# Kernel tuning notes

Hardware: AMD Instinct MI355X
Metric: run time of the kernel (lower is better)

The kernel has to match this reference:

```python
import jax, jax.numpy as jnp
import numpy as np
import math
from functools import lru_cache

# ---------- Clebsch-Gordan machinery (numpy, setup-time only) ----------

def _cg(j1, m1, j2, m2, j, m):
    """Complex-basis CG coefficient via Racah's formula (Condon-Shortley)."""
    if m1 + m2 != m:
        return 0.0
    f = math.factorial
    pre = (2 * j + 1) * f(j1 + j2 - j) * f(j1 - j2 + j) * f(-j1 + j2 + j) / f(j1 + j2 + j + 1)
    pre *= f(j1 + m1) * f(j1 - m1) * f(j2 + m2) * f(j2 - m2) * f(j + m) * f(j - m)
    s = 0.0
    for k in range(0, j1 + j2 - j + 1):
        d = (k, j1 + j2 - j - k, j1 - m1 - k, j2 + m2 - k, j - j2 + m1 + k, j - j1 - m2 + k)
        if min(d) < 0:
            continue
        s += (-1) ** k / (f(d[0]) * f(d[1]) * f(d[2]) * f(d[3]) * f(d[4]) * f(d[5]))
    return math.sqrt(pre) * s


def _csh_to_rsh(j):
    """Unitary complex->real spherical harmonics transform, columns indexed by real m."""
    C = np.zeros((2 * j + 1, 2 * j + 1), dtype=np.complex128)
    s2 = 1.0 / math.sqrt(2.0)
    for m in range(-j, j + 1):
        am = abs(m)
        if m < 0:
            C[j + m, j + m] = 1j * s2
            C[j - m, j + m] = -1j * ((-1) ** am) * s2
        elif m == 0:
            C[j, j] = 1.0
        else:
            C[j - m, j + m] = s2
            C[j + m, j + m] = ((-1) ** am) * s2
    return C


@lru_cache(maxsize=None)
def _rsh_cg(j1, j2, j):
    """Real-basis CG, compactified to rows [m1, m2, m, coeff] over nonzeros."""
    csh = np.zeros((2 * j1 + 1, 2 * j2 + 1, 2 * j + 1), dtype=np.complex128)
    for m1 in range(-j1, j1 + 1):
        for m2 in range(-j2, j2 + 1):
            m = m1 + m2
            if -j <= m <= j:
                csh[j1 + m1, j2 + m2, j + m] = _cg(j1, m1, j2, m2, j, m)
    r = np.einsum('abc,ai,bj,ck->ijk', csh, _csh_to_rsh(j1), _csh_to_rsh(j2), np.conj(_csh_to_rsh(j)))
    r = np.real(r * ((-1j) ** (j1 + j2 + j)))
    m1g, m2g, mg = np.meshgrid(np.arange(-j1, j1 + 1), np.arange(-j2, j2 + 1),
                               np.arange(-j, j + 1), indexing='ij')
    mask = np.abs(r) > 1e-12
    return np.stack([m1g[mask].astype(np.float64), m2g[mask].astype(np.float64),
                     mg[mask].astype(np.float64), r[mask]], axis=0)


def _build_coupler(md1, md2, trunc_in=True):
    """Faithful replay of CGPCoupler._init_params: returns cg_tilde, repids, out_dim."""
    md1 = np.asarray(md1, dtype=np.int64)
    md2 = np.asarray(md2, dtype=np.int64)
    md_in = np.stack([md1, md2], axis=0)                      # [2, 2*(L+1)]
    max_n_out = np.maximum(md1, md2)
    nlp = md_in.shape[1]
    n_irr = np.repeat(np.arange(nlp // 2) * 2 + 1, 2)         # irreps per (l,p) slot
    off_in = np.cumsum(md_in * n_irr[None, :], axis=1)
    off_in = np.concatenate([np.zeros((2, 1), dtype=np.int64), off_in[:, :-1]], axis=1)
    max_l = nlp // 2 - 1
    md_out = np.zeros_like(max_n_out)
    valid = []
    for lout in range(max_l + 1):
        for pout in (1, -1):
            for l1 in range(max_l + 1):
                for l2 in range(max_l + 1):
                    for p1 in (1, -1):
                        for p2 in (1, -1):
                            cp = (-1) ** (lout + l1 + l2)
                            if p1 * p2 * cp != pout:
                                continue
                            if l1 + l2 < lout or abs(l1 - l2) > lout:
                                continue
                            lp1 = 2 * l1 + (1 - p1) // 2
                            lp2 = 2 * l2 + (1 - p2) // 2
                            lpo = 2 * lout + (1 - pout) // 2
                            if trunc_in:
                                if l1 + l2 > max_l:
                                    continue
                                deg = min(md_in[0, lp1], md_in[1, lp2],
                                          max_n_out[2 * (l1 + l2) + (1 - pout) // 2])
                            else:
                                deg = min(md_in[0, lp1], md_in[1, lp2], max_n_out[lpo])
                            md_out[lpo] += deg
                            if deg > 0:
                                valid.append((lpo, lp1, lp2, int(deg)))
    off_out = np.cumsum(md_out * n_irr)
    off_out = np.concatenate([[0], off_out[:-1]]).astype(np.int64)
    cg_l, r1_l, r2_l, ro_l = [], [], [], []
    ns_off, lpo_last = 0, 0
    for lpo, lp1, lp2, deg in valid:
        if lpo > lpo_last:
            ns_off = 0
        l1, l2, lout = lp1 // 2, lp2 // 2, lpo // 2
        src = _rsh_cg(l1, l2, lout)                            # [4, nnz]
        seg = np.repeat(src, deg, axis=1)                      # repeat_interleave along dim=1
        ns = np.tile(np.arange(deg, dtype=np.int64), src.shape[1])
        r1_l.append(off_in[0, lp1] + np.rint(seg[0] + l1).astype(np.int64) * md_in[0, lp1] + ns)
        r2_l.append(off_in[1, lp2] + np.rint(seg[1] + l2).astype(np.int64) * md_in[1, lp2] + ns)
        ro_l.append(off_out[lpo] + np.rint(seg[2] + lout).astype(np.int64) * md_out[lpo] + ns_off + ns)
        cg_l.append(seg[3])
        ns_off += deg
        lpo_last = lpo
    out_dim = int(np.sum(md_out * n_irr))
    return (np.concatenate(cg_l), np.concatenate(r1_l), np.concatenate(r2_l),
            np.concatenate(ro_l), out_dim)


METADATA = [32, 32, 32, 32, 32, 32, 32, 32]   # max_l = 3, 32 channels per (l, parity)
BATCH = 2048


def setup_inputs() -> dict:
    key = jax.random.key(0)
    k1, k2 = jax.random.split(key)
    cg, r1, r2, ro, out_dim = _build_coupler(METADATA, METADATA, trunc_in=True)
    n_irr = np.repeat(np.arange(len(METADATA) // 2) * 2 + 1, 2)
    in_dim = int(np.sum(np.asarray(METADATA) * n_irr))        # 1024
    x1 = jax.random.normal(k1, (BATCH, in_dim), dtype=jnp.float32)
    x2 = jax.random.normal(k2, (BATCH, in_dim), dtype=jnp.float32)
    return {
        "x1": x1,
        "x2": x2,
        "cg_tilde": jnp.asarray(cg, dtype=jnp.float32),
        "repids_in1": jnp.asarray(r1, dtype=jnp.int64) if jax.config.jax_enable_x64 else jnp.asarray(r1, dtype=jnp.int32),
        "repids_in2": jnp.asarray(r2, dtype=jnp.int64) if jax.config.jax_enable_x64 else jnp.asarray(r2, dtype=jnp.int32),
        "repids_out": jnp.asarray(ro, dtype=jnp.int64) if jax.config.jax_enable_x64 else jnp.asarray(ro, dtype=jnp.int32),
        "out_dim": out_dim,
    }


def reference(x1, x2, cg_tilde, repids_in1, repids_in2, repids_out, out_dim):
    # gather along rep dim (last), elementwise multiply with CG coeffs, scatter-add
    out_tilde = x1[:, repids_in1] * x2[:, repids_in2] * cg_tilde[None, :]   # [B, K]
    out = jnp.zeros((x1.shape[0], out_dim), dtype=x1.dtype).at[:, repids_out].add(out_tilde)
    return out
```

## Files before the change

### kernel.cpp

```cpp
#include <hip/hip_runtime.h>


#define IN_DIM  1024
#define ROWS    8
#define NOBCAP  512
#define SKIP_OB 511u

__global__ __launch_bounds__(1024) void prep_kernel(
    const int* __restrict__ r1, const int* __restrict__ r2,
    const int* __restrict__ ro, const float* __restrict__ cg,
    int nseg, int nob,
    uint2* __restrict__ qdesc, uint2* __restrict__ ddesc, uint2* __restrict__ sdesc,
    int* __restrict__ zlist, int* __restrict__ hdr)
{
    __shared__ int cntS[NOBCAP], rankS[NOBCAP];
    __shared__ int qoffS[NOBCAP], doffS[NOBCAP], soffS[NOBCAP];
    __shared__ unsigned long long wsumS[8], woffS[8];
    const int t = threadIdx.x;

    if (t < NOBCAP) { cntS[t] = 0; rankS[t] = 0; }
    __syncthreads();

    for (int s = t; s < nseg; s += 1024)
        atomicAdd(&cntS[ro[s << 5] >> 5], 1);
    __syncthreads();

    int c = 0;
    unsigned long long pv = 0ull;
    if (t < NOBCAP) {
        c = (t < nob) ? cntS[t] : 0;
        unsigned long long q = 0, df = 0, sf = 0, zf = 0;
        if (t < nob) {
            if (c == 2)      df = 1;
            else if (c <= 1) sf = 1;
            else { q = (unsigned long long)((c + 3) >> 2); if (c > 4) zf = 1; }
        }
        pv = (q << 48) | (df << 32) | (sf << 16) | zf;
    }
    const int lane = t & 63;
    const int wid  = t >> 6;
    #pragma unroll
    for (int off = 1; off < 64; off <<= 1) {
        const unsigned long long n = __shfl_up(pv, off, 64);
        if (lane >= off) pv += n;
    }
    if (t < NOBCAP && lane == 63) wsumS[wid] = pv;
    __syncthreads();
    if (t < 8) {
        unsigned long long v = wsumS[t];
        const unsigned long long self = v;
        #pragma unroll
        for (int off = 1; off < 8; off <<= 1) {
            const unsigned long long n = __shfl_up(v, off, 64);
            if (t >= off) v += n;
        }
        woffS[t] = v - self;
    }
    __syncthreads();

    if (t < NOBCAP) {
        const unsigned long long incl = pv + woffS[wid];
        const int qi = (int)(incl >> 48);
        const int di = (int)((incl >> 32) & 0xFFFFull);
        const int si = (int)((incl >> 16) & 0xFFFFull);
        const int zi = (int)(incl & 0xFFFFull);
        if (t < nob) {
            if (c == 2) {
                doffS[t] = di - 1;
            } else if (c <= 1) {
                soffS[t] = si - 1;
                if (c == 0)
                    sdesc[si - 1] = make_uint2(((unsigned int)t << 20) | 0x80000000u, 0u);
            } else {
                const int qn = (c + 3) >> 2;
                const int qb = qi - qn;
                qoffS[t] = qb;
                const unsigned int fl = (c > 4) ? 0u : 0x80000000u;
                if (c > 4) zlist[zi - 1] = t;
                const unsigned int pd = ((unsigned int)t << 20) | fl;
                for (int j = (qb << 2) + c; j < ((qb + qn) << 2); ++j)
                    qdesc[j] = make_uint2(pd, 0u);
            }
        }
        if (t == NOBCAP - 1) {
            const int nq = qi, nd = di, ns = si;
            const int nqPad = (nq + 15) & ~15;
            const int ndPad = (nd + 31) & ~31;
            const int nsPad = (ns + 63) & ~63;
            const uint2 dummy = make_uint2(SKIP_OB << 20, 0u);
            for (int j = (nq << 2); j < (nqPad << 2); ++j) qdesc[j] = dummy;
            for (int j = (nd << 1); j < (ndPad << 1); ++j) ddesc[j] = dummy;
            for (int j = ns;        j < nsPad;        ++j) sdesc[j] = dummy;
            hdr[0] = nqPad; hdr[1] = zi; hdr[2] = ndPad; hdr[3] = nsPad;
        }
    }
    __syncthreads();

    for (int s = t; s < nseg; s += 1024) {
        const int k  = s << 5;
        const int ob = ro[k] >> 5;
        const int cc = cntS[ob];
        const int rk = atomicAdd(&rankS[ob], 1);
        const unsigned int fl = (cc > 4) ? 0u : 0x80000000u;
        const uint2 v = make_uint2((unsigned int)r1[k] | ((unsigned int)r2[k] << 10)
                                   | ((unsigned int)ob << 20) | fl,
                                   __float_as_uint(cg[k]));
        if (cc == 2)      ddesc[(doffS[ob] << 1) + rk] = v;
        else if (cc == 1) sdesc[soffS[ob]] = v;
        else              qdesc[(qoffS[ob] << 2) + rk] = v;
    }
}

__device__ __forceinline__ void accum4(float4& acc, unsigned int dx, unsigned int dc,
                                       const float* xs1, const float* xs2)
{
    const float  c = __uint_as_float(dc);
    const float4 u = *reinterpret_cast<const float4*>(xs1 + (dx & 1023u));
    const float4 v = *reinterpret_cast<const float4*>(xs2 + ((dx >> 10) & 1023u));
    acc.x = fmaf(c, u.x * v.x, acc.x);
    acc.y = fmaf(c, u.y * v.y, acc.y);
    acc.z = fmaf(c, u.z * v.z, acc.z);
    acc.w = fmaf(c, u.w * v.w, acc.w);
}

__device__ __forceinline__ void terminal(float* orow, unsigned int hx, float4 acc)
{
    const int ob = (int)((hx >> 20) & 511u);
    if (ob == (int)SKIP_OB) return;
    float* p = orow + (ob << 5);
    if (hx >> 31) {
        *reinterpret_cast<float4*>(p) = acc;
    } else {
        unsafeAtomicAdd(p,     acc.x);
        unsafeAtomicAdd(p + 1, acc.y);
        unsafeAtomicAdd(p + 2, acc.z);
        unsafeAtomicAdd(p + 3, acc.w);
    }
}

__global__ __launch_bounds__(1024) void cgp_main(const float* __restrict__ x1,
    const float* __restrict__ x2, const uint2* __restrict__ qdesc,
    const uint2* __restrict__ ddesc, const uint2* __restrict__ sdesc,
    const int* __restrict__ zlist, const int* __restrict__ hdr,
    float* __restrict__ out, int out_dim)
{
    __shared__ float x1s[ROWS * IN_DIM];
    __shared__ float x2s[ROWS * IN_DIM];
    const int r0  = blockIdx.x * ROWS;
    const int tid = threadIdx.x;

    {
        const float4* p1 = reinterpret_cast<const float4*>(x1 + (size_t)r0 * IN_DIM);
        const float4* p2 = reinterpret_cast<const float4*>(x2 + (size_t)r0 * IN_DIM);
        float4* s1 = reinterpret_cast<float4*>(x1s);
        float4* s2 = reinterpret_cast<float4*>(x2s);
        #pragma unroll
        for (int j = tid; j < (ROWS * IN_DIM) >> 2; j += 1024) { s1[j] = p1[j]; s2[j] = p2[j]; }
    }
    const int nz = hdr[1];
    for (int i = tid; i < (nz << 5); i += 1024) {
        const int ob = zlist[i >> 5];
        const int ch = i & 31;
        float* p = out + (size_t)r0 * out_dim + (ob << 5) + ch;
        #pragma unroll
        for (int j = 0; j < ROWS; ++j) p[j * out_dim] = 0.f;
    }
    __syncthreads();

    const int w  = tid >> 6;
    const int ln = tid & 63;
    const int rr = ln >> 3;
    const int tt = ln & 7;
    const float* xs1 = x1s + rr * IN_DIM + (tt << 2);
    const float* xs2 = x2s + rr * IN_DIM + (tt << 2);
    float* orow = out + (size_t)(r0 + rr) * out_dim + (tt << 2);

    {
        const int qpw = hdr[0] >> 4;
        const uint2* qd = qdesc + ((size_t)(w * qpw) << 2);
        #pragma unroll 2
        for (int i = 0; i < qpw; ++i, qd += 4) {
            const uint4 A  = *reinterpret_cast<const uint4*>(qd);
            const uint4 Bq = *reinterpret_cast<const uint4*>(qd + 2);
            float4 acc = make_float4(0.f, 0.f, 0.f, 0.f);
            accum4(acc, A.x,  A.y,  xs1, xs2);
            accum4(acc, A.z,  A.w,  xs1, xs2);
            accum4(acc, Bq.x, Bq.y, xs1, xs2);
            accum4(acc, Bq.z, Bq.w, xs1, xs2);
            terminal(orow, A.x, acc);
        }
    }

    {
        const int ppw = hdr[2] >> 5;
        const uint2* dd = ddesc + ((size_t)(w * ppw) << 2);
        #pragma unroll 2
        for (int i = 0; i < ppw; ++i, dd += 4) {
            const uint4 A  = *reinterpret_cast<const uint4*>(dd);
            const uint4 Bq = *reinterpret_cast<const uint4*>(dd + 2);
            float4 a0 = make_float4(0.f, 0.f, 0.f, 0.f);
            float4 a1 = make_float4(0.f, 0.f, 0.f, 0.f);
            accum4(a0, A.x,  A.y,  xs1, xs2);
            accum4(a0, A.z,  A.w,  xs1, xs2);
            accum4(a1, Bq.x, Bq.y, xs1, xs2);
            accum4(a1, Bq.z, Bq.w, xs1, xs2);
            terminal(orow, A.x,  a0);
            terminal(orow, Bq.x, a1);
        }
    }

    {
        const int spw = hdr[3] >> 4;
        const int ipw = spw >> 2;
        const uint2* sd = sdesc + (size_t)(w * spw);
        #pragma unroll 2
        for (int i = 0; i < ipw; ++i, sd += 4) {
            const uint4 A  = *reinterpret_cast<const uint4*>(sd);
            const uint4 Bq = *reinterpret_cast<const uint4*>(sd + 2);
            float4 a0 = make_float4(0.f, 0.f, 0.f, 0.f);
            float4 a1 = make_float4(0.f, 0.f, 0.f, 0.f);
            float4 a2 = make_float4(0.f, 0.f, 0.f, 0.f);
            float4 a3 = make_float4(0.f, 0.f, 0.f, 0.f);
            accum4(a0, A.x,  A.y,  xs1, xs2);
            accum4(a1, A.z,  A.w,  xs1, xs2);
            accum4(a2, Bq.x, Bq.y, xs1, xs2);
            accum4(a3, Bq.z, Bq.w, xs1, xs2);
            terminal(orow, A.x,  a0);
            terminal(orow, A.z,  a1);
            terminal(orow, Bq.x, a2);
            terminal(orow, Bq.z, a3);
        }
    }
}

extern "C" void kernel_launch(void* const* d_in, const int* in_sizes, int n_in,
                              void* d_out, int out_size, void* d_ws, size_t ws_size,
                              hipStream_t stream)
{
    const float* x1 = (const float*)d_in[0];
    const float* x2 = (const float*)d_in[1];
    const float* cg = (const float*)d_in[2];
    const int*   r1 = (const int*)d_in[3];
    const int*   r2 = (const int*)d_in[4];
    const int*   ro = (const int*)d_in[5];
    float* out = (float*)d_out;

    const int B       = in_sizes[0] / IN_DIM;
    const int out_dim = out_size / B;
    const int K       = in_sizes[2];
    const int nseg    = K >> 5;
    const int nob     = out_dim >> 5;
    const int qcap    = nob + (nseg >> 2) + 32;
    const int dcap    = nob + 48;
    const int scap    = nob + 80;

    auto align16 = [](size_t v) { return (v + 15) & ~(size_t)15; };
    char* ws = (char*)d_ws;
    uint2* qdesc = (uint2*)ws;  ws += align16((size_t)qcap * 4 * sizeof(uint2));
    uint2* ddesc = (uint2*)ws;  ws += align16((size_t)dcap * 2 * sizeof(uint2));
    uint2* sdesc = (uint2*)ws;  ws += align16((size_t)scap * sizeof(uint2));
    int*   zlist = (int*)ws;    ws += align16((size_t)NOBCAP * sizeof(int));
    int*   hdr   = (int*)ws;

    hipLaunchKernelGGL(prep_kernel, dim3(1), dim3(1024), 0, stream,
                       r1, r2, ro, cg, nseg, nob, qdesc, ddesc, sdesc, zlist, hdr);
    hipLaunchKernelGGL(cgp_main, dim3(B / ROWS), dim3(1024), 0, stream,
                       x1, x2, qdesc, ddesc, sdesc, zlist, hdr, out, out_dim);
}
```

Measured before the change: 28.87 us.

## Halve rows per block and split each wave into two half-waves on different descriptors

```diff
diff --git a/kernel.cpp b/kernel.cpp
--- a/kernel.cpp
+++ b/kernel.cpp
@@ -2,7 +2,7 @@
 
 
 #define IN_DIM  1024
-#define ROWS    8
+#define ROWS    4
 #define NOBCAP  512
 #define SKIP_OB 511u
 
@@ -138,7 +138,7 @@
     }
 }
 
-__global__ __launch_bounds__(1024) void cgp_main(const float* __restrict__ x1,
+__global__ __launch_bounds__(512) void cgp_main(const float* __restrict__ x1,
     const float* __restrict__ x2, const uint2* __restrict__ qdesc,
     const uint2* __restrict__ ddesc, const uint2* __restrict__ sdesc,
     const int* __restrict__ zlist, const int* __restrict__ hdr,
@@ -155,10 +155,10 @@
         float4* s1 = reinterpret_cast<float4*>(x1s);
         float4* s2 = reinterpret_cast<float4*>(x2s);
         #pragma unroll
-        for (int j = tid; j < (ROWS * IN_DIM) >> 2; j += 1024) { s1[j] = p1[j]; s2[j] = p2[j]; }
+        for (int j = tid; j < (ROWS * IN_DIM) >> 2; j += 512) { s1[j] = p1[j]; s2[j] = p2[j]; }
     }
     const int nz = hdr[1];
-    for (int i = tid; i < (nz << 5); i += 1024) {
+    for (int i = tid; i < (nz << 5); i += 512) {
         const int ob = zlist[i >> 5];
         const int ch = i & 31;
         float* p = out + (size_t)r0 * out_dim + (ob << 5) + ch;
@@ -169,19 +169,24 @@
 
     const int w  = tid >> 6;
     const int ln = tid & 63;
-    const int rr = ln >> 3;
-    const int tt = ln & 7;
+    const bool hi = (ln >> 5) != 0;
+    const int hl = ln & 31;
+    const int rr = hl >> 3;
+    const int tt = hl & 7;
     const float* xs1 = x1s + rr * IN_DIM + (tt << 2);
     const float* xs2 = x2s + rr * IN_DIM + (tt << 2);
     float* orow = out + (size_t)(r0 + rr) * out_dim + (tt << 2);
 
     {
-        const int qpw = hdr[0] >> 4;
+        const int qpw = hdr[0] >> 3;
         const uint2* qd = qdesc + ((size_t)(w * qpw) << 2);
-        #pragma unroll 2
-        for (int i = 0; i < qpw; ++i, qd += 4) {
-            const uint4 A  = *reinterpret_cast<const uint4*>(qd);
-            const uint4 Bq = *reinterpret_cast<const uint4*>(qd + 2);
+        for (int i = 0; i < qpw; i += 2, qd += 8) {
+            const uint4 A0 = *reinterpret_cast<const uint4*>(qd);
+            const uint4 B0 = *reinterpret_cast<const uint4*>(qd + 2);
+            const uint4 A1 = *reinterpret_cast<const uint4*>(qd + 4);
+            const uint4 B1 = *reinterpret_cast<const uint4*>(qd + 6);
+            const uint4 A  = hi ? A1 : A0;
+            const uint4 Bq = hi ? B1 : B0;
             float4 acc = make_float4(0.f, 0.f, 0.f, 0.f);
             accum4(acc, A.x,  A.y,  xs1, xs2);
             accum4(acc, A.z,  A.w,  xs1, xs2);
@@ -192,12 +197,15 @@
     }
 
     {
-        const int ppw = hdr[2] >> 5;
-        const uint2* dd = ddesc + ((size_t)(w * ppw) << 2);
-        #pragma unroll 2
-        for (int i = 0; i < ppw; ++i, dd += 4) {
-            const uint4 A  = *reinterpret_cast<const uint4*>(dd);
-            const uint4 Bq = *reinterpret_cast<const uint4*>(dd + 2);
+        const int dpw = hdr[2] >> 3;
+        const uint2* dd = ddesc + ((size_t)(w * dpw) << 1);
+        for (int i = 0; i < dpw; i += 4, dd += 8) {
+            const uint4 A0 = *reinterpret_cast<const uint4*>(dd);
+            const uint4 B0 = *reinterpret_cast<const uint4*>(dd + 2);
+            const uint4 A1 = *reinterpret_cast<const uint4*>(dd + 4);
+            const uint4 B1 = *reinterpret_cast<const uint4*>(dd + 6);
+            const uint4 A  = hi ? A1 : A0;
+            const uint4 Bq = hi ? B1 : B0;
             float4 a0 = make_float4(0.f, 0.f, 0.f, 0.f);
             float4 a1 = make_float4(0.f, 0.f, 0.f, 0.f);
             accum4(a0, A.x,  A.y,  xs1, xs2);
@@ -210,13 +218,15 @@
     }
 
     {
-        const int spw = hdr[3] >> 4;
-        const int ipw = spw >> 2;
+        const int spw = hdr[3] >> 3;
         const uint2* sd = sdesc + (size_t)(w * spw);
-        #pragma unroll 2
-        for (int i = 0; i < ipw; ++i, sd += 4) {
-            const uint4 A  = *reinterpret_cast<const uint4*>(sd);
-            const uint4 Bq = *reinterpret_cast<const uint4*>(sd + 2);
+        for (int i = 0; i < spw; i += 8, sd += 8) {
+            const uint4 A0 = *reinterpret_cast<const uint4*>(sd);
+            const uint4 B0 = *reinterpret_cast<const uint4*>(sd + 2);
+            const uint4 A1 = *reinterpret_cast<const uint4*>(sd + 4);
+            const uint4 B1 = *reinterpret_cast<const uint4*>(sd + 6);
+            const uint4 A  = hi ? A1 : A0;
+            const uint4 Bq = hi ? B1 : B0;
             float4 a0 = make_float4(0.f, 0.f, 0.f, 0.f);
             float4 a1 = make_float4(0.f, 0.f, 0.f, 0.f);
             float4 a2 = make_float4(0.f, 0.f, 0.f, 0.f);
@@ -264,6 +274,6 @@
 
     hipLaunchKernelGGL(prep_kernel, dim3(1), dim3(1024), 0, stream,
                        r1, r2, ro, cg, nseg, nob, qdesc, ddesc, sdesc, zlist, hdr);
-    hipLaunchKernelGGL(cgp_main, dim3(B / ROWS), dim3(1024), 0, stream,
+    hipLaunchKernelGGL(cgp_main, dim3(B / ROWS), dim3(512), 0, stream,
                        x1, x2, qdesc, ddesc, sdesc, zlist, hdr, out, out_dim);
 }
```

Result: slower. 29.74 us (+3.0%).
